# Optimization experiments

Measured on AMD Instinct MI355X. Metric: run time of the kernel, lower is better.

## Reference

```python
import jax, jax.numpy as jnp
import numpy as np

GRID_SIZE = 5
SPLINE_ORDER = 3
GRID_RANGE = (-1.0, 1.0)


def b_splines(x, grid, spline_order=SPLINE_ORDER):
    # x: [B, in], grid: [G] with G = grid_size + 2*spline_order + 1
    x = x[..., None]                      # [B, in, 1]
    g = grid[None, None, :]               # [1, 1, G]
    bases = ((x >= g[..., :-1]) & (x < g[..., 1:])).astype(x.dtype)  # [B, in, G-1]
    for k in range(1, spline_order + 1):
        left = (x - g[..., :-(k + 1)]) / (g[..., k:-1] - g[..., :-(k + 1)]) * bases[..., :-1]
        right = (g[..., k + 1:] - x) / (g[..., k + 1:] - g[..., 1:-k]) * bases[..., 1:]
        bases = left + right
    return bases                          # [B, in, grid_size + spline_order]


def setup_inputs() -> dict:
    key = jax.random.key(0)
    k1, k2, k3, k4 = jax.random.split(key, 4)
    B, IN, OUT = 32768, 256, 256
    n_coef = GRID_SIZE + SPLINE_ORDER  # 8
    h = (GRID_RANGE[1] - GRID_RANGE[0]) / GRID_SIZE
    grid = jnp.arange(-SPLINE_ORDER, GRID_SIZE + SPLINE_ORDER + 1, dtype=jnp.float32) * h + GRID_RANGE[0]  # [12]
    x = jax.random.normal(k1, (B, IN), dtype=jnp.float32)
    base_weight = jax.random.normal(k2, (OUT, IN), dtype=jnp.float32) * np.sqrt(2.0 / IN)
    spline_weight = jax.random.normal(k3, (OUT, IN, n_coef), dtype=jnp.float32) * (0.1 / GRID_SIZE)
    spline_scaler = jax.random.normal(k4, (OUT, IN), dtype=jnp.float32) * np.sqrt(2.0 / IN)
    return {"x": x, "base_weight": base_weight, "spline_weight": spline_weight,
            "spline_scaler": spline_scaler, "grid": grid}


def reference(x, base_weight, spline_weight, spline_scaler, grid):
    B = x.shape[0]
    out_features = base_weight.shape[0]
    # base branch: silu(x) @ base_weight^T
    base_out = jnp.matmul(jax.nn.silu(x), base_weight.T)  # [B, out]
    # spline branch
    bases = b_splines(x, grid)                             # [B, in, n_coef]
    scaled_w = spline_weight * spline_scaler[..., None]    # [out, in, n_coef]
    spline_out = jnp.matmul(bases.reshape(B, -1), scaled_w.reshape(out_features, -1).T)
    return base_out + spline_out
```

## Files before the change

kernel.cpp:

```cpp
#include <hip/hip_runtime.h>
#include <hip/hip_bf16.h>
#include <stdint.h>


#define IN_F 256
#define OUT_F 256
#define KDIM 2304
#define BK 64
#define NCHUNK (KDIM / BK)
#define TBINS 512
#define WC_BYTES ((size_t)OUT_F * KDIM * 2)

#define AS1 __attribute__((address_space(1)))
#define AS3 __attribute__((address_space(3)))

typedef float f32x4 __attribute__((ext_vector_type(4)));
typedef short bf16x8 __attribute__((ext_vector_type(8)));

__device__ __forceinline__ uint32_t f2bf(float f) {
    union { float f; uint32_t u; } c; c.f = f;
    uint32_t u = c.u;
    return (u + 0x7FFFu + ((u >> 16) & 1u)) >> 16;
}

__device__ __forceinline__ float silu_f(float v) {
    return v / (1.0f + __expf(-v));
}

__global__ void build_w(const float* __restrict__ bw, const float* __restrict__ sw,
                        const float* __restrict__ ss, unsigned short* __restrict__ Wc,
                        uint64_t* __restrict__ tg) {
    const int o = blockIdx.x;
    const int i = threadIdx.x;
    Wc[o * KDIM + i] = (unsigned short)f2bf(bw[o * IN_F + i]);
    const float scal = ss[o * IN_F + i];
    const float4* swv = reinterpret_cast<const float4*>(sw + (size_t)(o * IN_F + i) * 8);
    float4 s0 = swv[0], s1 = swv[1];
    uint4 wv;
    wv.x = f2bf(s0.x * scal) | (f2bf(s0.y * scal) << 16);
    wv.y = f2bf(s0.z * scal) | (f2bf(s0.w * scal) << 16);
    wv.z = f2bf(s1.x * scal) | (f2bf(s1.y * scal) << 16);
    wv.w = f2bf(s1.z * scal) | (f2bf(s1.w * scal) << 16);
    *reinterpret_cast<uint4*>(Wc + o * KDIM + IN_F + i * 8) = wv;

    if (o == 0) {
        for (int k = i; k < TBINS; k += IN_F) {
            float t = (k + 0.5f) * (1.0f / TBINS);
            float t2 = t * t, t3 = t2 * t;
            float p3 = t3 * (1.0f / 6.0f);
            float p2 = -0.5f * t3 + 0.5f * t2 + 0.5f * t + (1.0f / 6.0f);
            float p1 = 0.5f * t3 - t2 + (2.0f / 3.0f);
            float omt = 1.0f - t;
            float p0 = omt * omt * omt * (1.0f / 6.0f);
            tg[k] = (uint64_t)f2bf(p0) | ((uint64_t)f2bf(p1) << 16) |
                    ((uint64_t)f2bf(p2) << 32) | ((uint64_t)f2bf(p3) << 48);
        }
    }
}

__launch_bounds__(512, 4)
__global__ void kan_fused(const float* __restrict__ x, const unsigned short* __restrict__ Wc,
                          const uint64_t* __restrict__ tg, float* __restrict__ out) {
    __shared__ __align__(16) unsigned short As[2][128 * 64];
    __shared__ __align__(16) unsigned short Bs[2][128 * 64];

    const int bid = blockIdx.x;
    const int row0 = (bid >> 1) * 128;
    const int col0 = (bid & 1) * 128;
    const int tid = threadIdx.x;
    const int lane = tid & 63;
    const int w = tid >> 6;
    const int wm = w >> 2;
    const int wn = w & 3;
    const int l15 = lane & 15;
    const int q = lane >> 4;

    const int sr = lane >> 3;
    const int s  = lane & 7;
    const int g  = s ^ sr;
    const int srow = w * 16 + sr;

    f32x4 acc[4][2] = {};
    float xr[2][8];
    uint64_t pk2[2];
    int j02[2];

    auto stage_b = [&](int kc, int buf) {
#pragma unroll
        for (int j = 0; j < 2; ++j) {
            const unsigned short* gp =
                Wc + (size_t)(col0 + srow + j * 8) * KDIM + kc * BK + g * 8;
            __builtin_amdgcn_global_load_lds((const AS1 void*)gp,
                                             (AS3 void*)&Bs[buf][(w * 16 + j * 8) * 64],
                                             16, 0, 0);
        }
    };
    auto load_x = [&](int kc) {
        if (kc < 4) {
#pragma unroll
            for (int j = 0; j < 2; ++j) {
                const float* xp = x + (size_t)(row0 + srow + j * 8) * IN_F + kc * 64 + g * 8;
                float4 a = *reinterpret_cast<const float4*>(xp);
                float4 b = *reinterpret_cast<const float4*>(xp + 4);
                xr[j][0] = a.x; xr[j][1] = a.y; xr[j][2] = a.z; xr[j][3] = a.w;
                xr[j][4] = b.x; xr[j][5] = b.y; xr[j][6] = b.z; xr[j][7] = b.w;
            }
        } else {
            const int i0 = (kc - 4) * 8 + g;
#pragma unroll
            for (int j = 0; j < 2; ++j) {
                float xx = x[(size_t)(row0 + srow + j * 8) * IN_F + i0];
                float u = __builtin_fmaf(xx, 2.5f, 5.5f);
                float jf = floorf(u);
                int bin = (int)((u - jf) * (float)TBINS) & (TBINS - 1);
                j02[j] = (int)jf;
                pk2[j] = tg[bin];
            }
        }
    };
    auto write_a = [&](int kc, int buf) {
        if (kc < 4) {
#pragma unroll
            for (int j = 0; j < 2; ++j) {
                uint4 wv;
                wv.x = f2bf(silu_f(xr[j][0])) | (f2bf(silu_f(xr[j][1])) << 16);
                wv.y = f2bf(silu_f(xr[j][2])) | (f2bf(silu_f(xr[j][3])) << 16);
                wv.z = f2bf(silu_f(xr[j][4])) | (f2bf(silu_f(xr[j][5])) << 16);
                wv.w = f2bf(silu_f(xr[j][6])) | (f2bf(silu_f(xr[j][7])) << 16);
                *reinterpret_cast<uint4*>(&As[buf][(srow + j * 8) * 64 + s * 8]) = wv;
            }
        } else {
#pragma unroll
            for (int j = 0; j < 2; ++j) {
                int j0 = j02[j];
                uint64_t pk = ((unsigned)j0 <= 10u) ? pk2[j] : 0ull;
                int jc = j0 < 0 ? 0 : (j0 > 10 ? 10 : j0);
                int sh = jc * 16 - 48;
                unsigned __int128 v = (unsigned __int128)pk;
                v = (sh >= 0) ? (v << sh) : (v >> (-sh));
                uint4 wv;
                wv.x = (uint32_t)v;
                wv.y = (uint32_t)(v >> 32);
                wv.z = (uint32_t)(v >> 64);
                wv.w = (uint32_t)(v >> 96);
                *reinterpret_cast<uint4*>(&As[buf][(srow + j * 8) * 64 + s * 8]) = wv;
            }
        }
    };

    stage_b(0, 0);
    load_x(0);
    write_a(0, 0);
    __syncthreads();

    for (int kc = 0; kc < NCHUNK; ++kc) {
        const int cur = kc & 1;
        const int nxt = cur ^ 1;
        if (kc + 1 < NCHUNK) {
            stage_b(kc + 1, nxt);
            load_x(kc + 1);
        }
#pragma unroll
        for (int kk = 0; kk < BK; kk += 32) {
            bf16x8 af[4], bfv[2];
            const int g0 = (kk >> 3) + q;
#pragma unroll
            for (int mt = 0; mt < 4; ++mt) {
                int r = wm * 64 + mt * 16 + l15;
                af[mt] = *reinterpret_cast<const bf16x8*>(
                    &As[cur][r * 64 + ((g0 ^ (r & 7)) << 3)]);
            }
#pragma unroll
            for (int nt = 0; nt < 2; ++nt) {
                int r = wn * 32 + nt * 16 + l15;
                bfv[nt] = *reinterpret_cast<const bf16x8*>(
                    &Bs[cur][r * 64 + ((g0 ^ (r & 7)) << 3)]);
            }
#pragma unroll
            for (int mt = 0; mt < 4; ++mt)
#pragma unroll
                for (int nt = 0; nt < 2; ++nt)
                    acc[mt][nt] = __builtin_amdgcn_mfma_f32_16x16x32_bf16(
                        af[mt], bfv[nt], acc[mt][nt], 0, 0, 0);
        }
        if (kc + 1 < NCHUNK) write_a(kc + 1, nxt);
        __syncthreads();
    }

#pragma unroll
    for (int mt = 0; mt < 4; ++mt) {
        int row = row0 + wm * 64 + mt * 16 + q * 4;
#pragma unroll
        for (int nt = 0; nt < 2; ++nt) {
            int col = col0 + wn * 32 + nt * 16 + l15;
#pragma unroll
            for (int r = 0; r < 4; ++r)
                out[(size_t)(row + r) * OUT_F + col] = acc[mt][nt][r];
        }
    }
}

extern "C" void kernel_launch(void* const* d_in, const int* in_sizes, int n_in,
                              void* d_out, int out_size, void* d_ws, size_t ws_size,
                              hipStream_t stream) {
    const float* x  = (const float*)d_in[0];
    const float* bw = (const float*)d_in[1];
    const float* sw = (const float*)d_in[2];
    const float* ss = (const float*)d_in[3];
    unsigned short* Wc = (unsigned short*)d_ws;
    uint64_t* tg = (uint64_t*)((char*)d_ws + WC_BYTES);

    build_w<<<dim3(OUT_F), dim3(IN_F), 0, stream>>>(bw, sw, ss, Wc, tg);

    const int B_ROWS = in_sizes[0] / IN_F;
    kan_fused<<<dim3(B_ROWS / 128 * 2), dim3(512), 0, stream>>>(x, Wc, tg, (float*)d_out);
}
```

Before: 146.9 us.

## Load A fragments directly into registers via full 8-wide basis lookup table

Drops the shared-memory A tile entirely. Each lane now builds its MFMA A fragments straight in registers: silu values are loaded from x for the base chunks, and for spline chunks a precomputed table of full 8-coefficient bf16 vectors (1410 entries, 128 bins per knot interval) is indexed by the clamped x value. This removes LDS writes and reads and the 128-bit shift logic for A. The main loop is also unrolled by two with ping-pong buffers. In exchange, the table lookups become scattered global or L2 reads, register pressure rises, and basis values are quantized to 128 bins per interval instead of 512.

```diff
diff --git a/kernel.cpp b/kernel.cpp
--- a/kernel.cpp
+++ b/kernel.cpp
@@ -7,8 +7,8 @@
 #define OUT_F 256
 #define KDIM 2304
 #define BK 64
-#define NCHUNK (KDIM / BK)
-#define TBINS 512
+#define NCHUNK 36
+#define TENT 1410
 #define WC_BYTES ((size_t)OUT_F * KDIM * 2)
 
 #define AS1 __attribute__((address_space(1)))
@@ -16,6 +16,8 @@
 
 typedef float f32x4 __attribute__((ext_vector_type(4)));
 typedef short bf16x8 __attribute__((ext_vector_type(8)));
+
+union U4B8 { uint4 u; bf16x8 v; };
 
 __device__ __forceinline__ uint32_t f2bf(float f) {
     union { float f; uint32_t u; } c; c.f = f;
@@ -29,7 +31,7 @@
 
 __global__ void build_w(const float* __restrict__ bw, const float* __restrict__ sw,
                         const float* __restrict__ ss, unsigned short* __restrict__ Wc,
-                        uint64_t* __restrict__ tg) {
+                        uint4* __restrict__ T) {
     const int o = blockIdx.x;
     const int i = threadIdx.x;
     Wc[o * KDIM + i] = (unsigned short)f2bf(bw[o * IN_F + i]);
@@ -44,25 +46,95 @@
     *reinterpret_cast<uint4*>(Wc + o * KDIM + IN_F + i * 8) = wv;
 
     if (o == 0) {
-        for (int k = i; k < TBINS; k += IN_F) {
-            float t = (k + 0.5f) * (1.0f / TBINS);
-            float t2 = t * t, t3 = t2 * t;
-            float p3 = t3 * (1.0f / 6.0f);
-            float p2 = -0.5f * t3 + 0.5f * t2 + 0.5f * t + (1.0f / 6.0f);
-            float p1 = 0.5f * t3 - t2 + (2.0f / 3.0f);
-            float omt = 1.0f - t;
-            float p0 = omt * omt * omt * (1.0f / 6.0f);
-            tg[k] = (uint64_t)f2bf(p0) | ((uint64_t)f2bf(p1) << 16) |
-                    ((uint64_t)f2bf(p2) << 32) | ((uint64_t)f2bf(p3) << 48);
+        for (int e = i; e < TENT; e += IN_F) {
+            uint4 ent = make_uint4(0, 0, 0, 0);
+            if (e > 0 && e < 1409) {
+                int v = e - 1;
+                int j0 = v >> 7;
+                float t = ((v & 127) + 0.5f) * (1.0f / 128.0f);
+                float t2 = t * t, t3 = t2 * t;
+                float p3 = t3 * (1.0f / 6.0f);
+                float p2 = -0.5f * t3 + 0.5f * t2 + 0.5f * t + (1.0f / 6.0f);
+                float p1 = 0.5f * t3 - t2 + (2.0f / 3.0f);
+                float omt = 1.0f - t;
+                float p0 = omt * omt * omt * (1.0f / 6.0f);
+                uint32_t h[8];
+                for (int j = 0; j < 8; ++j) {
+                    int sdx = j0 - j;
+                    float val = (sdx == 0) ? p3 : (sdx == 1) ? p2
+                              : (sdx == 2) ? p1 : (sdx == 3) ? p0 : 0.0f;
+                    h[j] = f2bf(val);
+                }
+                ent.x = h[0] | (h[1] << 16);
+                ent.y = h[2] | (h[3] << 16);
+                ent.z = h[4] | (h[5] << 16);
+                ent.w = h[6] | (h[7] << 16);
+            }
+            T[e] = ent;
         }
     }
 }
 
+#define TBL_IDX(xx, dst) { \
+    float _u = __builtin_fmaf((xx), 320.0f, 704.0f); \
+    _u = fminf(fmaxf(_u, -1.0f), 1408.0f); \
+    dst = (int)floorf(_u) + 1; }
+
+#define STAGE_B(KC1, BSN) { \
+    __builtin_amdgcn_global_load_lds((const AS1 void*)(wbase0 + (KC1) * 128), \
+        (AS3 void*)&BSN[ldst0], 16, 0, 0); \
+    __builtin_amdgcn_global_load_lds((const AS1 void*)(wbase1 + (KC1) * 128), \
+        (AS3 void*)&BSN[ldst1], 16, 0, 0); }
+
+#define PREFETCH_A(KC1, AFN) { \
+    const int _i0 = ((KC1) - 4) * 8; \
+    _Pragma("unroll") \
+    for (int _mt = 0; _mt < 4; ++_mt) { \
+      float _x0 = xbq[_mt * 4096 + _i0]; \
+      float _x1 = xbq[_mt * 4096 + _i0 + 4]; \
+      int _t0, _t1; \
+      TBL_IDX(_x0, _t0) \
+      TBL_IDX(_x1, _t1) \
+      AFN[_mt] = T8[_t0]; \
+      AFN[_mt + 4] = T8[_t1]; \
+    } }
+
+#define CHUNK(KC, BSC, BSN, AFC, AFN) { \
+    if ((KC) + 1 < NCHUNK) { \
+      STAGE_B((KC) + 1, BSN) \
+      if ((KC) + 1 >= 4) PREFETCH_A((KC) + 1, AFN) \
+    } \
+    if ((KC) < 4) { \
+      _Pragma("unroll") \
+      for (int _f = 0; _f < 8; ++_f) { \
+        const float* _xp = xsl + (_f & 3) * 4096 + (KC) * 64 + (_f >> 2) * 32; \
+        float4 _a = *(const float4*)_xp; \
+        float4 _b = *(const float4*)(_xp + 4); \
+        U4B8 _c; \
+        _c.u.x = f2bf(silu_f(_a.x)) | (f2bf(silu_f(_a.y)) << 16); \
+        _c.u.y = f2bf(silu_f(_a.z)) | (f2bf(silu_f(_a.w)) << 16); \
+        _c.u.z = f2bf(silu_f(_b.x)) | (f2bf(silu_f(_b.y)) << 16); \
+        _c.u.w = f2bf(silu_f(_b.z)) | (f2bf(silu_f(_b.w)) << 16); \
+        AFC[_f] = _c.v; \
+      } \
+    } \
+    _Pragma("unroll") \
+    for (int _ks = 0; _ks < 2; ++_ks) { \
+      bf16x8 _b0 = *(const bf16x8*)((const char*)BSC + boff[_ks * 2 + 0]); \
+      bf16x8 _b1 = *(const bf16x8*)((const char*)BSC + boff[_ks * 2 + 1]); \
+      _Pragma("unroll") \
+      for (int _mt = 0; _mt < 4; ++_mt) { \
+        acc[_mt][0] = __builtin_amdgcn_mfma_f32_16x16x32_bf16(AFC[_mt + 4 * _ks], _b0, acc[_mt][0], 0, 0, 0); \
+        acc[_mt][1] = __builtin_amdgcn_mfma_f32_16x16x32_bf16(AFC[_mt + 4 * _ks], _b1, acc[_mt][1], 0, 0, 0); \
+      } \
+    } \
+    __syncthreads(); }
+
 __launch_bounds__(512, 4)
 __global__ void kan_fused(const float* __restrict__ x, const unsigned short* __restrict__ Wc,
-                          const uint64_t* __restrict__ tg, float* __restrict__ out) {
-    __shared__ __align__(16) unsigned short As[2][128 * 64];
-    __shared__ __align__(16) unsigned short Bs[2][128 * 64];
+                          const bf16x8* __restrict__ T8, float* __restrict__ out) {
+    __shared__ __align__(16) unsigned short Bs0[128 * 64];
+    __shared__ __align__(16) unsigned short Bs1[128 * 64];
 
     const int bid = blockIdx.x;
     const int row0 = (bid >> 1) * 128;
@@ -76,115 +148,38 @@
     const int q = lane >> 4;
 
     const int sr = lane >> 3;
-    const int s  = lane & 7;
-    const int g  = s ^ sr;
+    const int s = lane & 7;
+    const int g = s ^ sr;
     const int srow = w * 16 + sr;
 
+    const char* wbase0 = (const char*)(Wc + (size_t)(col0 + srow) * KDIM + g * 8);
+    const char* wbase1 = (const char*)(Wc + (size_t)(col0 + srow + 8) * KDIM + g * 8);
+    const int ldst0 = (w * 16) * 64;
+    const int ldst1 = (w * 16 + 8) * 64;
+
+    const float* xbq = x + (size_t)(row0 + wm * 64 + l15) * IN_F + q;
+    const float* xsl = x + (size_t)(row0 + wm * 64 + l15) * IN_F + q * 8;
+
+    int boff[4];
+#pragma unroll
+    for (int ks = 0; ks < 2; ++ks)
+#pragma unroll
+        for (int nt = 0; nt < 2; ++nt) {
+            int r = wn * 32 + nt * 16 + l15;
+            boff[ks * 2 + nt] = r * 128 + (((ks * 4 + q) ^ (l15 & 7)) << 4);
+        }
+
     f32x4 acc[4][2] = {};
-    float xr[2][8];
-    uint64_t pk2[2];
-    int j02[2];
-
-    auto stage_b = [&](int kc, int buf) {
-#pragma unroll
-        for (int j = 0; j < 2; ++j) {
-            const unsigned short* gp =
-                Wc + (size_t)(col0 + srow + j * 8) * KDIM + kc * BK + g * 8;
-            __builtin_amdgcn_global_load_lds((const AS1 void*)gp,
-                                             (AS3 void*)&Bs[buf][(w * 16 + j * 8) * 64],
-                                             16, 0, 0);
-        }
-    };
-    auto load_x = [&](int kc) {
-        if (kc < 4) {
-#pragma unroll
-            for (int j = 0; j < 2; ++j) {
-                const float* xp = x + (size_t)(row0 + srow + j * 8) * IN_F + kc * 64 + g * 8;
-                float4 a = *reinterpret_cast<const float4*>(xp);
-                float4 b = *reinterpret_cast<const float4*>(xp + 4);
-                xr[j][0] = a.x; xr[j][1] = a.y; xr[j][2] = a.z; xr[j][3] = a.w;
-                xr[j][4] = b.x; xr[j][5] = b.y; xr[j][6] = b.z; xr[j][7] = b.w;
-            }
-        } else {
-            const int i0 = (kc - 4) * 8 + g;
-#pragma unroll
-            for (int j = 0; j < 2; ++j) {
-                float xx = x[(size_t)(row0 + srow + j * 8) * IN_F + i0];
-                float u = __builtin_fmaf(xx, 2.5f, 5.5f);
-                float jf = floorf(u);
-                int bin = (int)((u - jf) * (float)TBINS) & (TBINS - 1);
-                j02[j] = (int)jf;
-                pk2[j] = tg[bin];
-            }
-        }
-    };
-    auto write_a = [&](int kc, int buf) {
-        if (kc < 4) {
-#pragma unroll
-            for (int j = 0; j < 2; ++j) {
-                uint4 wv;
-                wv.x = f2bf(silu_f(xr[j][0])) | (f2bf(silu_f(xr[j][1])) << 16);
-                wv.y = f2bf(silu_f(xr[j][2])) | (f2bf(silu_f(xr[j][3])) << 16);
-                wv.z = f2bf(silu_f(xr[j][4])) | (f2bf(silu_f(xr[j][5])) << 16);
-                wv.w = f2bf(silu_f(xr[j][6])) | (f2bf(silu_f(xr[j][7])) << 16);
-                *reinterpret_cast<uint4*>(&As[buf][(srow + j * 8) * 64 + s * 8]) = wv;
-            }
-        } else {
-#pragma unroll
-            for (int j = 0; j < 2; ++j) {
-                int j0 = j02[j];
-                uint64_t pk = ((unsigned)j0 <= 10u) ? pk2[j] : 0ull;
-                int jc = j0 < 0 ? 0 : (j0 > 10 ? 10 : j0);
-                int sh = jc * 16 - 48;
-                unsigned __int128 v = (unsigned __int128)pk;
-                v = (sh >= 0) ? (v << sh) : (v >> (-sh));
-                uint4 wv;
-                wv.x = (uint32_t)v;
-                wv.y = (uint32_t)(v >> 32);
-                wv.z = (uint32_t)(v >> 64);
-                wv.w = (uint32_t)(v >> 96);
-                *reinterpret_cast<uint4*>(&As[buf][(srow + j * 8) * 64 + s * 8]) = wv;
-            }
-        }
-    };
-
-    stage_b(0, 0);
-    load_x(0);
-    write_a(0, 0);
+    bf16x8 afA[8], afB[8];
+
+    STAGE_B(0, Bs0)
     __syncthreads();
 
-    for (int kc = 0; kc < NCHUNK; ++kc) {
-        const int cur = kc & 1;
-        const int nxt = cur ^ 1;
-        if (kc + 1 < NCHUNK) {
-            stage_b(kc + 1, nxt);
-            load_x(kc + 1);
-        }
-#pragma unroll
-        for (int kk = 0; kk < BK; kk += 32) {
-            bf16x8 af[4], bfv[2];
-            const int g0 = (kk >> 3) + q;
-#pragma unroll
-            for (int mt = 0; mt < 4; ++mt) {
-                int r = wm * 64 + mt * 16 + l15;
-                af[mt] = *reinterpret_cast<const bf16x8*>(
-                    &As[cur][r * 64 + ((g0 ^ (r & 7)) << 3)]);
-            }
-#pragma unroll
-            for (int nt = 0; nt < 2; ++nt) {
-                int r = wn * 32 + nt * 16 + l15;
-                bfv[nt] = *reinterpret_cast<const bf16x8*>(
-                    &Bs[cur][r * 64 + ((g0 ^ (r & 7)) << 3)]);
-            }
-#pragma unroll
-            for (int mt = 0; mt < 4; ++mt)
-#pragma unroll
-                for (int nt = 0; nt < 2; ++nt)
-                    acc[mt][nt] = __builtin_amdgcn_mfma_f32_16x16x32_bf16(
-                        af[mt], bfv[nt], acc[mt][nt], 0, 0, 0);
-        }
-        if (kc + 1 < NCHUNK) write_a(kc + 1, nxt);
-        __syncthreads();
+#pragma unroll 1
+    for (int it = 0; it < NCHUNK / 2; ++it) {
+        const int kc0 = it * 2;
+        CHUNK(kc0, Bs0, Bs1, afA, afB)
+        CHUNK(kc0 + 1, Bs1, Bs0, afB, afA)
     }
 
 #pragma unroll
@@ -208,10 +203,11 @@
     const float* sw = (const float*)d_in[2];
     const float* ss = (const float*)d_in[3];
     unsigned short* Wc = (unsigned short*)d_ws;
-    uint64_t* tg = (uint64_t*)((char*)d_ws + WC_BYTES);
-
-    build_w<<<dim3(OUT_F), dim3(IN_F), 0, stream>>>(bw, sw, ss, Wc, tg);
+    uint4* T = (uint4*)((char*)d_ws + WC_BYTES);
+
+    build_w<<<dim3(OUT_F), dim3(IN_F), 0, stream>>>(bw, sw, ss, Wc, T);
 
     const int B_ROWS = in_sizes[0] / IN_F;
-    kan_fused<<<dim3(B_ROWS / 128 * 2), dim3(512), 0, stream>>>(x, Wc, tg, (float*)d_out);
-}
+    kan_fused<<<dim3(B_ROWS / 128 * 2), dim3(512), 0, stream>>>(
+        x, Wc, (const bf16x8*)T, (float*)d_out);
+}
```

Measured after the change: 328.3 us. +123.4%, slower.
